# Kernel optimization log

Hardware: AMD Instinct MI355X
Metric: run time of the kernel (lower is better)

Reference implementation:

```python
import jax, jax.numpy as jnp
import numpy as np

N_NODES = 50000
N_EDGES = 800000
HIDDEN = 128
N_LAYERS = 3
MAX_Z = 1000
N_GRAPHS = 512
LN_EPS = 1e-5


def setup_inputs() -> dict:
    key = jax.random.key(0)
    ks = jax.random.split(key, 16)
    s = 0.05
    inp = {
        "z": jax.random.randint(ks[0], (N_NODES,), 0, MAX_Z),
        "edge_index": jax.random.randint(ks[1], (2, N_EDGES), 0, N_NODES),
        "batch": jnp.sort(jax.random.randint(ks[2], (N_NODES,), 0, N_GRAPHS)),
        "z_table": jax.random.normal(ks[3], (MAX_Z, HIDDEN), jnp.float32) * s,
        "W1": jax.random.normal(ks[4], (N_LAYERS, HIDDEN, HIDDEN), jnp.float32) * s,
        "b1": jnp.zeros((N_LAYERS, HIDDEN), jnp.float32),
        "W2": jax.random.normal(ks[5], (N_LAYERS, HIDDEN, HIDDEN), jnp.float32) * s,
        "b2": jnp.zeros((N_LAYERS, HIDDEN), jnp.float32),
        "ln_g": jnp.ones((N_LAYERS, HIDDEN), jnp.float32),
        "ln_b": jnp.zeros((N_LAYERS, HIDDEN), jnp.float32),
        "lin1_W": jax.random.normal(ks[6], (N_LAYERS * HIDDEN, HIDDEN), jnp.float32) * s,
        "lin1_b": jnp.zeros((HIDDEN,), jnp.float32),
        "lin2_W": jax.random.normal(ks[7], (HIDDEN, 1), jnp.float32) * s,
        "lin2_b": jnp.zeros((1,), jnp.float32),
    }
    return inp


def _layernorm(h, g, b):
    mu = jnp.mean(h, axis=-1, keepdims=True)
    var = jnp.mean((h - mu) ** 2, axis=-1, keepdims=True)
    return g * (h - mu) * jax.lax.rsqrt(var + LN_EPS) + b


def _gin_conv(x, src, dst, W1, b1, W2, b2, g, b):
    # sum-aggregate neighbor features, eps = 0 (train_eps=False)
    agg = jax.ops.segment_sum(x[src], dst, num_segments=N_NODES)
    h = x + agg
    h = jax.nn.relu(h @ W1 + b1)
    h = jax.nn.relu(h @ W2 + b2)
    return _layernorm(h, g, b)


def reference(z, edge_index, batch, z_table, W1, b1, W2, b2, ln_g, ln_b,
              lin1_W, lin1_b, lin2_W, lin2_b):
    src, dst = edge_index[0], edge_index[1]
    x = z_table[z]  # [N, H] z embedding (z is 1-D so no sum over dim 1)
    xs = []
    for l in range(N_LAYERS):
        x = _gin_conv(x, src, dst, W1[l], b1[l], W2[l], b2[l], ln_g[l], ln_b[l])
        xs.append(x)
    xcat = jnp.concatenate(xs, axis=1)  # JK concat [N, L*H]
    # global mean pool over graphs
    sums = jax.ops.segment_sum(xcat, batch, num_segments=N_GRAPHS)
    cnts = jax.ops.segment_sum(jnp.ones((N_NODES, 1), xcat.dtype), batch,
                               num_segments=N_GRAPHS)
    pooled = sums / jnp.maximum(cnts, 1.0)
    h = jax.nn.relu(pooled @ lin1_W + lin1_b)
    # dropout is identity in eval mode
    return h @ lin2_W + lin2_b  # [N_GRAPHS, 1]
```

## Files before the change

### kernel.cpp

```cpp
#include <hip/hip_runtime.h>
#include <hip/hip_bf16.h>

#define NN 50000
#define NE 800000
#define HD 128
#define NL 3
#define NG 512
#define LN_EPS 1e-5f

typedef unsigned short u16;
typedef unsigned int u32;
typedef __attribute__((ext_vector_type(8))) short short8;
typedef __attribute__((ext_vector_type(4))) float f32x4;

__device__ __forceinline__ u16 f2bf(float f){
  u32 x = __float_as_uint(f);
  u32 r = (x + 0x7fffu + ((x >> 16) & 1u)) >> 16;
  return (u16)r;
}
__device__ __forceinline__ float blo(u32 u){ return __uint_as_float(u << 16); }
__device__ __forceinline__ float bhi(u32 u){ return __uint_as_float(u & 0xffff0000u); }
__device__ __forceinline__ u32 pk2(float a, float b){ return (u32)f2bf(a) | ((u32)f2bf(b) << 16); }

__device__ __forceinline__ int lower_bound_dev(const int* a, int n, int v){
  int lo = 0, hi = n;
  while (lo < hi){ int m = (lo + hi) >> 1; if (a[m] < v) lo = m + 1; else hi = m; }
  return lo;
}

__global__ __launch_bounds__(256) void k_prep_w(const float* __restrict__ W1,
    const float* __restrict__ W2, u16* __restrict__ Wt){
  int t = blockIdx.x * 256 + threadIdx.x;
  if (t >= 6 * 128 * 128) return;
  int w = t >> 14, r = t & 16383, n = r >> 7, k = r & 127;
  int l = w >> 1;
  const float* Ws = (w & 1) ? (W2 + l * 16384) : (W1 + l * 16384);
  Wt[t] = f2bf(Ws[k * 128 + n]);
}

__global__ __launch_bounds__(256) void k_embed(const int* __restrict__ z,
    const float* __restrict__ tab, u16* __restrict__ xb){
  int gt = blockIdx.x * 256 + threadIdx.x;
  int node = gt >> 5, q = gt & 31;
  float4 v = *reinterpret_cast<const float4*>(tab + (size_t)z[node] * 128 + q * 4);
  uint2 p = { pk2(v.x, v.y), pk2(v.z, v.w) };
  *reinterpret_cast<uint2*>(xb + (size_t)node * 128 + q * 4) = p;
}

__global__ __launch_bounds__(256) void k_count(const int* __restrict__ dst,
    int* __restrict__ deg){
  int e = blockIdx.x * 256 + threadIdx.x;
  if (e < NE) atomicAdd(&deg[dst[e]], 1);
}

__global__ __launch_bounds__(256) void k_scan1(const int* __restrict__ deg,
    int* __restrict__ part, int* __restrict__ bsum){
  int i = blockIdx.x * 256 + threadIdx.x;
  int v = (i < NN) ? deg[i] : 0;
  int lane = threadIdx.x & 63, wave = threadIdx.x >> 6;
  int s = v;
  for (int off = 1; off < 64; off <<= 1){ int n = __shfl_up(s, off); if (lane >= off) s += n; }
  __shared__ int wsums[4];
  if (lane == 63) wsums[wave] = s;
  __syncthreads();
  int add = 0;
  for (int w = 0; w < wave; ++w) add += wsums[w];
  int incl = s + add;
  if (i < NN) part[i] = incl - v;
  if (threadIdx.x == 255) bsum[blockIdx.x] = incl;
}

__global__ __launch_bounds__(256) void k_scan2(int* __restrict__ bsum, int nb){
  int tid = threadIdx.x;
  int v = (tid < nb) ? bsum[tid] : 0;
  int lane = tid & 63, wave = tid >> 6;
  int s = v;
  for (int off = 1; off < 64; off <<= 1){ int n = __shfl_up(s, off); if (lane >= off) s += n; }
  __shared__ int wsums[4];
  if (lane == 63) wsums[wave] = s;
  __syncthreads();
  int add = 0;
  for (int w = 0; w < wave; ++w) add += wsums[w];
  int incl = s + add;
  if (tid < nb) bsum[tid] = incl - v;
}

__global__ __launch_bounds__(256) void k_scan3(const int* __restrict__ part,
    const int* __restrict__ bsum, int* __restrict__ rowptr, int* __restrict__ cursor){
  int i = blockIdx.x * 256 + threadIdx.x;
  if (i < NN){ int r = part[i] + bsum[blockIdx.x]; rowptr[i] = r; cursor[i] = r; }
  if (i == 0) rowptr[NN] = NE;
}

__global__ __launch_bounds__(256) void k_fill(const int* __restrict__ src,
    const int* __restrict__ dst, int* __restrict__ cursor, int* __restrict__ col){
  int e = blockIdx.x * 256 + threadIdx.x;
  if (e < NE){ int p = atomicAdd(&cursor[dst[e]], 1); col[p] = src[e]; }
}

__global__ __launch_bounds__(256) void k_gather(const int* __restrict__ rowptr,
    const int* __restrict__ col, const u16* __restrict__ xb, u16* __restrict__ hb){
  int wave = threadIdx.x >> 6, lane = threadIdx.x & 63;
  int node = blockIdx.x * 4 + wave;
  int q = lane >> 4, l4 = lane & 15;
  float a[8] = {0.f,0.f,0.f,0.f,0.f,0.f,0.f,0.f};
  float b[8] = {0.f,0.f,0.f,0.f,0.f,0.f,0.f,0.f};
  if (q == 0){
    uint4 s = *reinterpret_cast<const uint4*>(xb + (size_t)node * 128 + l4 * 8);
    a[0] = blo(s.x); a[1] = bhi(s.x); a[2] = blo(s.y); a[3] = bhi(s.y);
    a[4] = blo(s.z); a[5] = bhi(s.z); a[6] = blo(s.w); a[7] = bhi(s.w);
  }
  int lo = rowptr[node], hi = rowptr[node + 1];
  int e = lo + q;
  for (; e + 4 < hi; e += 8){
    int c0 = col[e], c1 = col[e + 4];
    uint4 v0 = *reinterpret_cast<const uint4*>(xb + (size_t)c0 * 128 + l4 * 8);
    uint4 v1 = *reinterpret_cast<const uint4*>(xb + (size_t)c1 * 128 + l4 * 8);
    a[0] += blo(v0.x); a[1] += bhi(v0.x); a[2] += blo(v0.y); a[3] += bhi(v0.y);
    a[4] += blo(v0.z); a[5] += bhi(v0.z); a[6] += blo(v0.w); a[7] += bhi(v0.w);
    b[0] += blo(v1.x); b[1] += bhi(v1.x); b[2] += blo(v1.y); b[3] += bhi(v1.y);
    b[4] += blo(v1.z); b[5] += bhi(v1.z); b[6] += blo(v1.w); b[7] += bhi(v1.w);
  }
  if (e < hi){
    int c0 = col[e];
    uint4 v0 = *reinterpret_cast<const uint4*>(xb + (size_t)c0 * 128 + l4 * 8);
    a[0] += blo(v0.x); a[1] += bhi(v0.x); a[2] += blo(v0.y); a[3] += bhi(v0.y);
    a[4] += blo(v0.z); a[5] += bhi(v0.z); a[6] += blo(v0.w); a[7] += bhi(v0.w);
  }
  #pragma unroll
  for (int j = 0; j < 8; ++j){
    a[j] += b[j];
    a[j] += __shfl_xor(a[j], 16);
    a[j] += __shfl_xor(a[j], 32);
  }
  if (q == 0){
    uint4 p = { pk2(a[0], a[1]), pk2(a[2], a[3]), pk2(a[4], a[5]), pk2(a[6], a[7]) };
    *reinterpret_cast<uint4*>(hb + (size_t)node * 128 + l4 * 8) = p;
  }
}

__global__ __launch_bounds__(256) void k_layer(const u16* __restrict__ A,
    const u16* __restrict__ Wt1, const u16* __restrict__ Wt2,
    const float* __restrict__ bias1, const float* __restrict__ bias2,
    const float* __restrict__ lng, const float* __restrict__ lnb,
    u16* __restrict__ Cout){
  __shared__ u16 As[128 * 128];
  __shared__ u16 Ws[128 * 128];
  int tid = threadIdx.x;
  int rb = blockIdx.x * 128;

  #pragma unroll
  for (int i = 0; i < 8; ++i){
    int u = tid + i * 256;
    int n = u >> 4, k8 = u & 15;
    uint4 w = *reinterpret_cast<const uint4*>(Wt1 + n * 128 + k8 * 8);
    *reinterpret_cast<uint4*>(&Ws[n * 128 + (k8 ^ (n & 15)) * 8]) = w;
  }
  #pragma unroll
  for (int i = 0; i < 8; ++i){
    int u = tid + i * 256;
    int row = u >> 4, k8 = u & 15;
    int grow = rb + row;
    uint4 v = {0u, 0u, 0u, 0u};
    if (grow < NN) v = *reinterpret_cast<const uint4*>(A + (size_t)grow * 128 + k8 * 8);
    *reinterpret_cast<uint4*>(&As[row * 128 + (k8 ^ (row & 15)) * 8]) = v;
  }
  __syncthreads();

  uint4 w2r[8];
  #pragma unroll
  for (int i = 0; i < 8; ++i){
    int u = tid + i * 256;
    int n = u >> 4, k8 = u & 15;
    w2r[i] = *reinterpret_cast<const uint4*>(Wt2 + n * 128 + k8 * 8);
  }

  int wave = tid >> 6, lane = tid & 63;
  int lrow = lane & 15, kgrp = lane >> 4;
  f32x4 acc[2][8];
  #pragma unroll
  for (int rt = 0; rt < 2; ++rt)
    #pragma unroll
    for (int nt = 0; nt < 8; ++nt) acc[rt][nt] = (f32x4){0.f, 0.f, 0.f, 0.f};

  #pragma unroll
  for (int ks = 0; ks < 4; ++ks){
    int ch = ks * 4 + kgrp;
    short8 a0 = *reinterpret_cast<const short8*>(&As[(wave * 32 + lrow) * 128 + (ch ^ lrow) * 8]);
    short8 a1 = *reinterpret_cast<const short8*>(&As[(wave * 32 + 16 + lrow) * 128 + (ch ^ lrow) * 8]);
    #pragma unroll
    for (int nt = 0; nt < 8; ++nt){
      short8 b = *reinterpret_cast<const short8*>(&Ws[(nt * 16 + lrow) * 128 + (ch ^ lrow) * 8]);
      acc[0][nt] = __builtin_amdgcn_mfma_f32_16x16x32_bf16(a0, b, acc[0][nt], 0, 0, 0);
      acc[1][nt] = __builtin_amdgcn_mfma_f32_16x16x32_bf16(a1, b, acc[1][nt], 0, 0, 0);
    }
  }

  #pragma unroll
  for (int nt = 0; nt < 8; ++nt){
    float bv = __ldg(bias1 + nt * 16 + lrow);
    #pragma unroll
    for (int rt = 0; rt < 2; ++rt)
      #pragma unroll
      for (int j = 0; j < 4; ++j)
        acc[rt][nt][j] = fmaxf(acc[rt][nt][j] + bv, 0.f);
  }

  __syncthreads();

  #pragma unroll
  for (int i = 0; i < 8; ++i){
    int u = tid + i * 256;
    int n = u >> 4, k8 = u & 15;
    *reinterpret_cast<uint4*>(&Ws[n * 128 + (k8 ^ (n & 15)) * 8]) = w2r[i];
  }
  #pragma unroll
  for (int rt = 0; rt < 2; ++rt)
    #pragma unroll
    for (int j = 0; j < 4; ++j){
      int row = wave * 32 + rt * 16 + kgrp * 4 + j;
      #pragma unroll
      for (int nt = 0; nt < 8; ++nt){
        int col = nt * 16 + lrow;
        int ch = (col >> 3) ^ (row & 15);
        As[row * 128 + ch * 8 + (col & 7)] = f2bf(acc[rt][nt][j]);
      }
    }
  __syncthreads();

  #pragma unroll
  for (int rt = 0; rt < 2; ++rt)
    #pragma unroll
    for (int nt = 0; nt < 8; ++nt) acc[rt][nt] = (f32x4){0.f, 0.f, 0.f, 0.f};

  #pragma unroll
  for (int ks = 0; ks < 4; ++ks){
    int ch = ks * 4 + kgrp;
    short8 a0 = *reinterpret_cast<const short8*>(&As[(wave * 32 + lrow) * 128 + (ch ^ lrow) * 8]);
    short8 a1 = *reinterpret_cast<const short8*>(&As[(wave * 32 + 16 + lrow) * 128 + (ch ^ lrow) * 8]);
    #pragma unroll
    for (int nt = 0; nt < 8; ++nt){
      short8 b = *reinterpret_cast<const short8*>(&Ws[(nt * 16 + lrow) * 128 + (ch ^ lrow) * 8]);
      acc[0][nt] = __builtin_amdgcn_mfma_f32_16x16x32_bf16(a0, b, acc[0][nt], 0, 0, 0);
      acc[1][nt] = __builtin_amdgcn_mfma_f32_16x16x32_bf16(a1, b, acc[1][nt], 0, 0, 0);
    }
  }

  float gv[8], lbv[8];
  #pragma unroll
  for (int nt = 0; nt < 8; ++nt){
    int gcol = nt * 16 + lrow;
    float bv = __ldg(bias2 + gcol);
    gv[nt] = __ldg(lng + gcol); lbv[nt] = __ldg(lnb + gcol);
    #pragma unroll
    for (int rt = 0; rt < 2; ++rt)
      #pragma unroll
      for (int j = 0; j < 4; ++j)
        acc[rt][nt][j] = fmaxf(acc[rt][nt][j] + bv, 0.f);
  }
  #pragma unroll
  for (int rt = 0; rt < 2; ++rt)
    #pragma unroll
    for (int j = 0; j < 4; ++j){
      float s = 0.f, sq = 0.f;
      #pragma unroll
      for (int nt = 0; nt < 8; ++nt){ float v = acc[rt][nt][j]; s += v; sq += v * v; }
      #pragma unroll
      for (int off = 1; off < 16; off <<= 1){
        s += __shfl_xor(s, off); sq += __shfl_xor(sq, off);
      }
      float mu = s * (1.f / 128.f);
      float var = sq * (1.f / 128.f) - mu * mu;
      float rstd = rsqrtf(var + LN_EPS);
      #pragma unroll
      for (int nt = 0; nt < 8; ++nt)
        acc[rt][nt][j] = gv[nt] * (acc[rt][nt][j] - mu) * rstd + lbv[nt];
    }

  #pragma unroll
  for (int rt = 0; rt < 2; ++rt){
    int rbase = rb + wave * 32 + rt * 16 + kgrp * 4;
    #pragma unroll
    for (int nt = 0; nt < 8; ++nt){
      int gcol = nt * 16 + lrow;
      #pragma unroll
      for (int j = 0; j < 4; ++j){
        int grow = rbase + j;
        if (grow < NN) Cout[(size_t)grow * 128 + gcol] = f2bf(acc[rt][nt][j]);
      }
    }
  }
}

__global__ __launch_bounds__(256) void k_pool(const u16* __restrict__ xb,
    const int* __restrict__ batch, float* __restrict__ pooled, int lslice){
  int g = blockIdx.x;
  int w = threadIdx.x >> 6, lane = threadIdx.x & 63;
  __shared__ float red[4][128];
  int lo = lower_bound_dev(batch, NN, g);
  int hi = lower_bound_dev(batch, NN, g + 1);
  float s0 = 0.f, s1 = 0.f;
  for (int i = lo + w; i < hi; i += 4){
    u32 u = *reinterpret_cast<const u32*>(xb + (size_t)i * 128 + lane * 2);
    s0 += blo(u); s1 += bhi(u);
  }
  red[w][lane * 2] = s0; red[w][lane * 2 + 1] = s1;
  __syncthreads();
  int f = threadIdx.x;
  if (f < 128)
    pooled[(size_t)g * 384 + lslice * 128 + f] = red[0][f] + red[1][f] + red[2][f] + red[3][f];
}

__global__ __launch_bounds__(128) void k_final(const float* __restrict__ pooled,
    const int* __restrict__ batch, const float* __restrict__ W1,
    const float* __restrict__ b1, const float* __restrict__ W2,
    const float* __restrict__ b2, float* __restrict__ out){
  int g = blockIdx.x, f = threadIdx.x;
  int lo = lower_bound_dev(batch, NN, g);
  int hi = lower_bound_dev(batch, NN, g + 1);
  float scale = 1.f / fmaxf((float)(hi - lo), 1.f);
  __shared__ float p[384];
  for (int k = f; k < 384; k += 128) p[k] = pooled[(size_t)g * 384 + k] * scale;
  __syncthreads();
  float acc = __ldg(b1 + f);
  for (int k = 0; k < 384; ++k) acc += p[k] * __ldg(W1 + k * 128 + f);
  float hval = fmaxf(acc, 0.f);
  float v = hval * __ldg(W2 + f);
  for (int off = 32; off; off >>= 1) v += __shfl_xor(v, off);
  __shared__ float red[2];
  int lane = f & 63, wave = f >> 6;
  if (lane == 0) red[wave] = v;
  __syncthreads();
  if (f == 0) out[g] = red[0] + red[1] + __ldg(b2);
}

extern "C" void kernel_launch(void* const* d_in, const int* in_sizes, int n_in,
                              void* d_out, int out_size, void* d_ws, size_t ws_size,
                              hipStream_t stream){
  const int*   z     = (const int*)d_in[0];
  const int*   ei    = (const int*)d_in[1];
  const int*   batch = (const int*)d_in[2];
  const float* ztab  = (const float*)d_in[3];
  const float* W1    = (const float*)d_in[4];
  const float* b1    = (const float*)d_in[5];
  const float* W2    = (const float*)d_in[6];
  const float* b2    = (const float*)d_in[7];
  const float* lng   = (const float*)d_in[8];
  const float* lnb   = (const float*)d_in[9];
  const float* l1W   = (const float*)d_in[10];
  const float* l1b   = (const float*)d_in[11];
  const float* l2W   = (const float*)d_in[12];
  const float* l2b   = (const float*)d_in[13];
  float* out = (float*)d_out;

  char* wsb = (char*)d_ws;
  size_t off = 0;
  auto alloc = [&](size_t bytes){ void* p = wsb + off; off += (bytes + 255) & ~(size_t)255; return p; };
  u16*   xbf    = (u16*)alloc((size_t)NN * 128 * 2);
  u16*   hbf    = (u16*)alloc((size_t)NN * 128 * 2);
  float* pooled = (float*)alloc((size_t)NG * 384 * 4);
  u16*   Wt     = (u16*)alloc((size_t)6 * 128 * 128 * 2);
  int*   deg    = (int*)alloc((size_t)NN * 4);
  int*   part   = (int*)alloc((size_t)NN * 4);
  int*   bsum   = (int*)alloc((size_t)256 * 4);
  int*   rowptr = (int*)alloc((size_t)(NN + 1) * 4);
  int*   cursor = (int*)alloc((size_t)NN * 4);
  int*   col    = (int*)alloc((size_t)NE * 4);

  const int* srcv = ei;
  const int* dstv = ei + NE;

  hipMemsetAsync(deg, 0, (size_t)NN * 4, stream);
  k_prep_w<<<(6 * 128 * 128 + 255) / 256, 256, 0, stream>>>(W1, W2, Wt);
  k_embed<<<NN * 32 / 256, 256, 0, stream>>>(z, ztab, xbf);
  k_count<<<(NE + 255) / 256, 256, 0, stream>>>(dstv, deg);
  int nb = (NN + 255) / 256;
  k_scan1<<<nb, 256, 0, stream>>>(deg, part, bsum);
  k_scan2<<<1, 256, 0, stream>>>(bsum, nb);
  k_scan3<<<nb, 256, 0, stream>>>(part, bsum, rowptr, cursor);
  k_fill<<<(NE + 255) / 256, 256, 0, stream>>>(srcv, dstv, cursor, col);

  int gb = (NN + 127) / 128;
  for (int l = 0; l < NL; ++l){
    k_gather<<<NN / 4, 256, 0, stream>>>(rowptr, col, xbf, hbf);
    k_layer<<<gb, 256, 0, stream>>>(hbf,
        Wt + (size_t)(l * 2 + 0) * 16384, Wt + (size_t)(l * 2 + 1) * 16384,
        b1 + l * 128, b2 + l * 128, lng + l * 128, lnb + l * 128, xbf);
    k_pool<<<NG, 256, 0, stream>>>(xbf, batch, pooled, l);
  }
  k_final<<<NG, 128, 0, stream>>>(pooled, batch, l1W, l1b, l2W, l2b, out);
}
```

Measured before the change: 424.5 us.

## Partition CSR build atomics by XCD node range and store column indices as u16

k_count and k_fill now use a fixed grid of 1024 blocks. Blocks are assigned to the 8 XCDs round-robin, and each one scans all edges but applies atomics only to destinations in its XCD's node slice. This keeps each counter's atomics on one XCD's L2 instead of bouncing between dies. The CSR column array is also stored as 16-bit indices, which halves index traffic in the three gather passes and relies on the node count staying below 65536. The cost is that every edge's dst is read 8 times, and the strided loop leaves fewer blocks in flight.

```diff
diff --git a/kernel.cpp b/kernel.cpp
--- a/kernel.cpp
+++ b/kernel.cpp
@@ -7,6 +7,8 @@
 #define NL 3
 #define NG 512
 #define LN_EPS 1e-5f
+#define NXCD 8
+#define NPX 6250
 
 typedef unsigned short u16;
 typedef unsigned int u32;
@@ -49,8 +51,13 @@
 
 __global__ __launch_bounds__(256) void k_count(const int* __restrict__ dst,
     int* __restrict__ deg){
-  int e = blockIdx.x * 256 + threadIdx.x;
-  if (e < NE) atomicAdd(&deg[dst[e]], 1);
+  int xcd = blockIdx.x & 7;
+  int grp = blockIdx.x >> 3;
+  int nlo = xcd * NPX, nhi = nlo + NPX;
+  for (int e = grp * 256 + threadIdx.x; e < NE; e += 128 * 256){
+    int d = dst[e];
+    if (d >= nlo && d < nhi) atomicAdd(&deg[d], 1);
+  }
 }
 
 __global__ __launch_bounds__(256) void k_scan1(const int* __restrict__ deg,
@@ -93,13 +100,21 @@
 }
 
 __global__ __launch_bounds__(256) void k_fill(const int* __restrict__ src,
-    const int* __restrict__ dst, int* __restrict__ cursor, int* __restrict__ col){
-  int e = blockIdx.x * 256 + threadIdx.x;
-  if (e < NE){ int p = atomicAdd(&cursor[dst[e]], 1); col[p] = src[e]; }
+    const int* __restrict__ dst, int* __restrict__ cursor, u16* __restrict__ col){
+  int xcd = blockIdx.x & 7;
+  int grp = blockIdx.x >> 3;
+  int nlo = xcd * NPX, nhi = nlo + NPX;
+  for (int e = grp * 256 + threadIdx.x; e < NE; e += 128 * 256){
+    int d = dst[e];
+    if (d >= nlo && d < nhi){
+      int p = atomicAdd(&cursor[d], 1);
+      col[p] = (u16)src[e];
+    }
+  }
 }
 
 __global__ __launch_bounds__(256) void k_gather(const int* __restrict__ rowptr,
-    const int* __restrict__ col, const u16* __restrict__ xb, u16* __restrict__ hb){
+    const u16* __restrict__ col, const u16* __restrict__ xb, u16* __restrict__ hb){
   int wave = threadIdx.x >> 6, lane = threadIdx.x & 63;
   int node = blockIdx.x * 4 + wave;
   int q = lane >> 4, l4 = lane & 15;
@@ -365,7 +380,7 @@
   int*   bsum   = (int*)alloc((size_t)256 * 4);
   int*   rowptr = (int*)alloc((size_t)(NN + 1) * 4);
   int*   cursor = (int*)alloc((size_t)NN * 4);
-  int*   col    = (int*)alloc((size_t)NE * 4);
+  u16*   col    = (u16*)alloc((size_t)NE * 2);
 
   const int* srcv = ei;
   const int* dstv = ei + NE;
@@ -373,12 +388,12 @@
   hipMemsetAsync(deg, 0, (size_t)NN * 4, stream);
   k_prep_w<<<(6 * 128 * 128 + 255) / 256, 256, 0, stream>>>(W1, W2, Wt);
   k_embed<<<NN * 32 / 256, 256, 0, stream>>>(z, ztab, xbf);
-  k_count<<<(NE + 255) / 256, 256, 0, stream>>>(dstv, deg);
+  k_count<<<1024, 256, 0, stream>>>(dstv, deg);
   int nb = (NN + 255) / 256;
   k_scan1<<<nb, 256, 0, stream>>>(deg, part, bsum);
   k_scan2<<<1, 256, 0, stream>>>(bsum, nb);
   k_scan3<<<nb, 256, 0, stream>>>(part, bsum, rowptr, cursor);
-  k_fill<<<(NE + 255) / 256, 256, 0, stream>>>(srcv, dstv, cursor, col);
+  k_fill<<<1024, 256, 0, stream>>>(srcv, dstv, cursor, col);
 
   int gb = (NN + 127) / 128;
   for (int l = 0; l < NL; ++l){
```

Result: faster. 410.8 us (-3.2%).
